# Optimization experiments

Hardware: AMD Instinct MI355X
Metric: run time of the kernel (lower is better)

Reference implementation:

```python
import jax, jax.numpy as jnp
import numpy as np

TEMPERATURE = 0.5
B, D = 4096, 256

def setup_inputs() -> dict:
    key = jax.random.key(0)
    k1, k2 = jax.random.split(key)
    z_i = jax.random.normal(k1, (B, D), dtype=jnp.float32)
    z_j = jax.random.normal(k2, (B, D), dtype=jnp.float32)
    return {"z_i": z_i, "z_j": z_j}

def reference(z_i, z_j):
    # NT-Xent loss (SimCLR). Cosine similarity of L2-normalized rows == dot product.
    b = z_i.shape[0]
    n = 2 * b
    zi = z_i / jnp.linalg.norm(z_i, axis=1, keepdims=True)
    zj = z_j / jnp.linalg.norm(z_j, axis=1, keepdims=True)
    z = jnp.concatenate([zi, zj], axis=0)            # [N, D]
    sim = jnp.matmul(z, z.T)                          # [N, N] cosine-sim matrix
    # positives: sim(i, i+b) and sim(i+b, i)
    pos = jnp.concatenate([jnp.diagonal(sim, offset=b), jnp.diagonal(sim, offset=-b)])  # [N]
    logits = sim / TEMPERATURE
    # Cross-entropy with the positive as the target class over {pos} U negatives.
    # The candidate set per row is all j != i (the positive j = partner(i) is included,
    # only the self-similarity diagonal is excluded) -> mask diagonal with -inf.
    neg_inf = jnp.asarray(-jnp.inf, dtype=logits.dtype)
    masked = jnp.where(jnp.eye(n, dtype=bool), neg_inf, logits)
    lse = jax.nn.logsumexp(masked, axis=1)            # [N]
    loss = jnp.sum(lse - pos / TEMPERATURE) / n
    return loss
```

## Files before the change

### kernel.cpp

```cpp
#include <hip/hip_runtime.h>
#include <hip/hip_bf16.h>


constexpr int BB = 4096;
constexpr int NN = 8192;
constexpr int DD = 256;
constexpr int TS = 128;
constexpr int NT = NN / TS;
constexpr int NBLK = NT * (NT + 1) / 2;
constexpr int KSTEPS = DD / 16;

typedef _Float16 half4v __attribute__((ext_vector_type(4)));
typedef _Float16 half8v __attribute__((ext_vector_type(8)));
typedef float floatx16 __attribute__((ext_vector_type(16)));

__global__ __launch_bounds__(256) void nt_normalize(
    const float* __restrict__ zi, const float* __restrict__ zj,
    _Float16* __restrict__ Zf, float* __restrict__ pos,
    float* __restrict__ rowsum)
{
    __shared__ _Float16 sZ[2][16 * 64 * 8];
    const int tid = threadIdx.x;
    const int pr  = tid >> 3;
    const int sub = tid & 7;
    const int p   = blockIdx.x * 32 + pr;

    if (blockIdx.x < 32) rowsum[blockIdx.x * 256 + tid] = 0.f;

    const float4* ai = (const float4*)(zi + (size_t)p * DD);
    const float4* bj = (const float4*)(zj + (size_t)p * DD);
    float4 av[8], bv[8];
    float ssi = 0.f, ssj = 0.f, dd = 0.f;
#pragma unroll
    for (int t = 0; t < 8; ++t) {
        av[t] = ai[sub + 8 * t];
        bv[t] = bj[sub + 8 * t];
        ssi += av[t].x*av[t].x + av[t].y*av[t].y + av[t].z*av[t].z + av[t].w*av[t].w;
        ssj += bv[t].x*bv[t].x + bv[t].y*bv[t].y + bv[t].z*bv[t].z + bv[t].w*bv[t].w;
        dd  += av[t].x*bv[t].x + av[t].y*bv[t].y + av[t].z*bv[t].z + av[t].w*bv[t].w;
    }
#pragma unroll
    for (int off = 1; off < 8; off <<= 1) {
        ssi += __shfl_xor(ssi, off);
        ssj += __shfl_xor(ssj, off);
        dd  += __shfl_xor(dd,  off);
    }
    const float invi = rsqrtf(ssi);
    const float invj = rsqrtf(ssj);
    if (sub == 0) pos[p] = dd * invi * invj;

#pragma unroll
    for (int t = 0; t < 8; ++t) {
        const int gi = (2 * t + (sub >> 2)) * 64 + pr + 32 * ((sub >> 1) & 1);
        const int wo = 4 * (sub & 1);
        half4v hi, hj;
        hi.x = (_Float16)(av[t].x * invi); hi.y = (_Float16)(av[t].y * invi);
        hi.z = (_Float16)(av[t].z * invi); hi.w = (_Float16)(av[t].w * invi);
        hj.x = (_Float16)(bv[t].x * invj); hj.y = (_Float16)(bv[t].y * invj);
        hj.z = (_Float16)(bv[t].z * invj); hj.w = (_Float16)(bv[t].w * invj);
        *(half4v*)&sZ[0][gi * 8 + wo] = hi;
        *(half4v*)&sZ[1][gi * 8 + wo] = hj;
    }
    __syncthreads();

    float4* Zf4 = (float4*)Zf;
    const float4* s0 = (const float4*)sZ[0];
    const float4* s1 = (const float4*)sZ[1];
    const size_t gbi = (size_t)blockIdx.x * 1024;
    const size_t gbj = (size_t)(128 + blockIdx.x) * 1024;
#pragma unroll
    for (int it = 0; it < 4; ++it) {
        Zf4[gbi + tid + it * 256] = s0[tid + it * 256];
        Zf4[gbj + tid + it * 256] = s1[tid + it * 256];
    }
}

__device__ __forceinline__ float half_sums(float x) {
    int t;
    t = __builtin_amdgcn_update_dpp(0, __builtin_bit_cast(int, x), 0x111, 0xf, 0xf, false);
    x += __builtin_bit_cast(float, t);
    t = __builtin_amdgcn_update_dpp(0, __builtin_bit_cast(int, x), 0x112, 0xf, 0xf, false);
    x += __builtin_bit_cast(float, t);
    t = __builtin_amdgcn_update_dpp(0, __builtin_bit_cast(int, x), 0x114, 0xf, 0xf, false);
    x += __builtin_bit_cast(float, t);
    t = __builtin_amdgcn_update_dpp(0, __builtin_bit_cast(int, x), 0x118, 0xf, 0xf, false);
    x += __builtin_bit_cast(float, t);
    t = __builtin_amdgcn_update_dpp(0, __builtin_bit_cast(int, x), 0x142, 0xa, 0xf, false);
    x += __builtin_bit_cast(float, t);
    return x;
}

__global__ __launch_bounds__(256, 4) void nt_simexp(
    const _Float16* __restrict__ Zf, float* __restrict__ rowsum)
{
    __shared__ float colacc[TS];

    const int bid = (blockIdx.x & 7) * (NBLK / 8) + (blockIdx.x >> 3);

    const int t = NBLK - 1 - bid;
    int m = (int)((sqrtf((float)(8 * t + 1)) - 1.0f) * 0.5f);
    while ((m + 1) * (m + 2) / 2 <= t) ++m;
    while (m * (m + 1) / 2 > t) --m;
    const int rt = NT - 1 - m;
    const int ct = NT - 1 - (t - m * (m + 1) / 2);
    const bool diag = (rt == ct);

    const int tid = threadIdx.x;
    const int wave = tid >> 6;
    const int lane = tid & 63;
    const int lm = lane & 31;
    const int lh = lane >> 5;
    const int wr = wave >> 1;
    const int wc = wave & 1;

    const int rbase = rt * TS;
    const int cbase = ct * TS;

    if (tid < TS) colacc[tid] = 0.f;
    __syncthreads();

    const int ga0 = (rbase >> 5) + wr * 2;
    const int gb0 = (cbase >> 5) + wc * 2;
    const half8v* pa0 = (const half8v*)Zf + (size_t)ga0 * 1024 + lane;
    const half8v* pa1 = pa0 + 1024;
    const half8v* pb0 = (const half8v*)Zf + (size_t)gb0 * 1024 + lane;
    const half8v* pb1 = pb0 + 1024;

    floatx16 a00, a01, a10, a11;
#pragma unroll
    for (int r = 0; r < 16; ++r) { a00[r] = 0.f; a01[r] = 0.f; a10[r] = 0.f; a11[r] = 0.f; }

    half8v fa0 = pa0[0], fa1 = pa1[0], fb0 = pb0[0], fb1 = pb1[0];
#pragma unroll
    for (int ks = 0; ks < KSTEPS; ++ks) {
        half8v na0 = fa0, na1 = fa1, nb0 = fb0, nb1 = fb1;
        if (ks + 1 < KSTEPS) {
            na0 = pa0[(ks + 1) * 64];
            na1 = pa1[(ks + 1) * 64];
            nb0 = pb0[(ks + 1) * 64];
            nb1 = pb1[(ks + 1) * 64];
        }
        a00 = __builtin_amdgcn_mfma_f32_32x32x16_f16(fa0, fb0, a00, 0, 0, 0);
        a01 = __builtin_amdgcn_mfma_f32_32x32x16_f16(fa0, fb1, a01, 0, 0, 0);
        a10 = __builtin_amdgcn_mfma_f32_32x32x16_f16(fa1, fb0, a10, 0, 0, 0);
        a11 = __builtin_amdgcn_mfma_f32_32x32x16_f16(fa1, fb1, a11, 0, 0, 0);
        fa0 = na0; fa1 = na1; fb0 = nb0; fb1 = nb1;
    }

    const float KEXP = 2.0f * 1.44269504088896340736f;
    float eb0 = 0.f, eb1 = 0.f;
#pragma unroll
    for (int tr = 0; tr < 2; ++tr) {
#pragma unroll
        for (int r = 0; r < 16; ++r) {
            const int mrow = (r & 3) + 8 * (r >> 2) + 4 * lh;
            float e0 = __builtin_amdgcn_exp2f((tr ? a10[r] : a00[r]) * KEXP);
            float e1 = __builtin_amdgcn_exp2f((tr ? a11[r] : a01[r]) * KEXP);
            if (diag && (wr == wc) && (mrow == lm)) {
                if (tr == 0) e0 = 0.f; else e1 = 0.f;
            }
            eb0 += e0; eb1 += e1;
            if (!diag) {
                float s2 = half_sums(e0 + e1);
                if (lm == 31)
                    atomicAdd(&colacc[wr * 64 + tr * 32 + mrow], s2);
            }
        }
    }

    eb0 += __shfl_xor(eb0, 32);
    eb1 += __shfl_xor(eb1, 32);
    if (lane < 32) {
        atomicAdd(&rowsum[cbase + wc * 64 + lm], eb0);
        atomicAdd(&rowsum[cbase + wc * 64 + 32 + lm], eb1);
    }
    if (!diag) {
        __syncthreads();
        if (tid < TS) atomicAdd(&rowsum[rbase + tid], colacc[tid]);
    }
}

__global__ __launch_bounds__(256) void nt_finalize(
    const float* __restrict__ rowsum, const float* __restrict__ pos,
    float* __restrict__ out)
{
    const int tid = threadIdx.x;
    float acc = 0.f;
#pragma unroll
    for (int it = 0; it < NN / 256; ++it)
        acc += __builtin_amdgcn_logf(rowsum[tid + it * 256]);
    float pacc = 0.f;
#pragma unroll
    for (int it = 0; it < BB / 256; ++it)
        pacc += pos[tid + it * 256];

#pragma unroll
    for (int off = 32; off > 0; off >>= 1) {
        acc  += __shfl_xor(acc,  off);
        pacc += __shfl_xor(pacc, off);
    }
    __shared__ float sa[4], sp[4];
    const int wave = tid >> 6;
    if ((tid & 63) == 0) { sa[wave] = acc; sp[wave] = pacc; }
    __syncthreads();
    if (tid == 0) {
        const float lntot = (sa[0] + sa[1] + sa[2] + sa[3]) * 0.6931471805599453f;
        const float ptot  = sp[0] + sp[1] + sp[2] + sp[3];
        out[0] = (lntot - 4.0f * ptot) * (1.0f / (float)NN);
    }
}

extern "C" void kernel_launch(void* const* d_in, const int* in_sizes, int n_in,
                              void* d_out, int out_size, void* d_ws, size_t ws_size,
                              hipStream_t stream) {
    const float* zi = (const float*)d_in[0];
    const float* zj = (const float*)d_in[1];
    float* out = (float*)d_out;

    _Float16* Zf = (_Float16*)d_ws;
    float* rowsum = (float*)((char*)d_ws + (size_t)NN * DD * 2);
    float* pos = rowsum + NN;

    nt_normalize<<<BB / 32, 256, 0, stream>>>(zi, zj, Zf, pos, rowsum);
    nt_simexp<<<NBLK, 256, 0, stream>>>((const _Float16*)Zf, rowsum);
    nt_finalize<<<1, 256, 0, stream>>>(rowsum, pos, out);
}
```

Measured before the change: 91.67 us.

## Stage row tile in LDS and sweep column chunks per block

Each block now loads a 128-row A tile into shared memory with global_load_lds. It then loops over up to eight column tiles of the upper triangle, with each wave computing a 128x64 strip, so A is reused across many column tiles instead of being reloaded from global memory for every 128x128 tile. Row-side partial sums are accumulated in shared memory and flushed once per block, which cuts global atomics. In exchange the grid shrinks to 288 blocks with uneven work (row chunks near the end are shorter), and register pressure rises with eight 32x32 accumulators per wave, hence the lower launch-bounds occupancy.

```diff
diff --git a/kernel.cpp b/kernel.cpp
--- a/kernel.cpp
+++ b/kernel.cpp
@@ -7,7 +7,8 @@
 constexpr int DD = 256;
 constexpr int TS = 128;
 constexpr int NT = NN / TS;
-constexpr int NBLK = NT * (NT + 1) / 2;
+constexpr int CW = 8;
+constexpr int NBLK = 288;
 constexpr int KSTEPS = DD / 16;
 
 typedef _Float16 half4v __attribute__((ext_vector_type(4)));
@@ -90,94 +91,118 @@
     return x;
 }
 
-__global__ __launch_bounds__(256, 4) void nt_simexp(
+__global__ __launch_bounds__(256, 2) void nt_simexp(
     const _Float16* __restrict__ Zf, float* __restrict__ rowsum)
 {
-    __shared__ float colacc[TS];
+    __shared__ alignas(16) _Float16 sA[4 * 16 * 64 * 8];
+    __shared__ float rowaccA[TS];
 
     const int bid = (blockIdx.x & 7) * (NBLK / 8) + (blockIdx.x >> 3);
 
-    const int t = NBLK - 1 - bid;
-    int m = (int)((sqrtf((float)(8 * t + 1)) - 1.0f) * 0.5f);
-    while ((m + 1) * (m + 2) / 2 <= t) ++m;
-    while (m * (m + 1) / 2 > t) --m;
-    const int rt = NT - 1 - m;
-    const int ct = NT - 1 - (t - m * (m + 1) / 2);
-    const bool diag = (rt == ct);
+    int rt = 0, rem = bid;
+    while (true) {
+        const int nch = (NT - rt + CW - 1) >> 3;
+        if (rem < nch) break;
+        rem -= nch; ++rt;
+    }
+    const int ct0 = rt + rem * CW;
+    const int ncw = min(CW, NT - ct0);
+    const int njobs = 2 * ncw;
 
     const int tid = threadIdx.x;
     const int wave = tid >> 6;
     const int lane = tid & 63;
     const int lm = lane & 31;
     const int lh = lane >> 5;
-    const int wr = wave >> 1;
-    const int wc = wave & 1;
-
-    const int rbase = rt * TS;
-    const int cbase = ct * TS;
-
-    if (tid < TS) colacc[tid] = 0.f;
-    __syncthreads();
-
-    const int ga0 = (rbase >> 5) + wr * 2;
-    const int gb0 = (cbase >> 5) + wc * 2;
-    const half8v* pa0 = (const half8v*)Zf + (size_t)ga0 * 1024 + lane;
-    const half8v* pa1 = pa0 + 1024;
-    const half8v* pb0 = (const half8v*)Zf + (size_t)gb0 * 1024 + lane;
-    const half8v* pb1 = pb0 + 1024;
-
-    floatx16 a00, a01, a10, a11;
-#pragma unroll
-    for (int r = 0; r < 16; ++r) { a00[r] = 0.f; a01[r] = 0.f; a10[r] = 0.f; a11[r] = 0.f; }
-
-    half8v fa0 = pa0[0], fa1 = pa1[0], fb0 = pb0[0], fb1 = pb1[0];
-#pragma unroll
-    for (int ks = 0; ks < KSTEPS; ++ks) {
-        half8v na0 = fa0, na1 = fa1, nb0 = fb0, nb1 = fb1;
-        if (ks + 1 < KSTEPS) {
-            na0 = pa0[(ks + 1) * 64];
-            na1 = pa1[(ks + 1) * 64];
-            nb0 = pb0[(ks + 1) * 64];
-            nb1 = pb1[(ks + 1) * 64];
-        }
-        a00 = __builtin_amdgcn_mfma_f32_32x32x16_f16(fa0, fb0, a00, 0, 0, 0);
-        a01 = __builtin_amdgcn_mfma_f32_32x32x16_f16(fa0, fb1, a01, 0, 0, 0);
-        a10 = __builtin_amdgcn_mfma_f32_32x32x16_f16(fa1, fb0, a10, 0, 0, 0);
-        a11 = __builtin_amdgcn_mfma_f32_32x32x16_f16(fa1, fb1, a11, 0, 0, 0);
-        fa0 = na0; fa1 = na1; fb0 = nb0; fb1 = nb1;
-    }
-
+
+    {
+        const _Float16* src = Zf + ((size_t)(rt * 4 + wave) * 1024 + lane) * 8;
+        _Float16* dst = sA + (size_t)wave * 16 * 64 * 8;
+#pragma unroll
+        for (int ks = 0; ks < 16; ++ks) {
+            __builtin_amdgcn_global_load_lds(
+                (const __attribute__((address_space(1))) unsigned int*)(src + ks * 64 * 8),
+                (__attribute__((address_space(3))) unsigned int*)(dst + ks * 64 * 8),
+                16, 0, 0);
+        }
+    }
+    if (tid < TS) rowaccA[tid] = 0.f;
+    __syncthreads();
+
+    const half8v* sAf = (const half8v*)sA;
     const float KEXP = 2.0f * 1.44269504088896340736f;
-    float eb0 = 0.f, eb1 = 0.f;
-#pragma unroll
-    for (int tr = 0; tr < 2; ++tr) {
-#pragma unroll
-        for (int r = 0; r < 16; ++r) {
-            const int mrow = (r & 3) + 8 * (r >> 2) + 4 * lh;
-            float e0 = __builtin_amdgcn_exp2f((tr ? a10[r] : a00[r]) * KEXP);
-            float e1 = __builtin_amdgcn_exp2f((tr ? a11[r] : a01[r]) * KEXP);
-            if (diag && (wr == wc) && (mrow == lm)) {
-                if (tr == 0) e0 = 0.f; else e1 = 0.f;
+
+    for (int j = wave; j < njobs; j += 4) {
+        const int ct = ct0 + (j >> 1);
+        const int jit = j & 1;
+        const bool dj = (ct == rt);
+        const int cb = ct * TS + jit * 64;
+
+        const half8v* pb0 = (const half8v*)Zf + ((size_t)(cb >> 5)) * 1024 + lane;
+        const half8v* pb1 = pb0 + 1024;
+
+        floatx16 acc[4][2];
+#pragma unroll
+        for (int g = 0; g < 4; ++g)
+#pragma unroll
+            for (int c = 0; c < 2; ++c)
+#pragma unroll
+                for (int r = 0; r < 16; ++r) acc[g][c][r] = 0.f;
+
+        half8v fb0 = pb0[0], fb1 = pb1[0];
+#pragma unroll
+        for (int ks = 0; ks < KSTEPS; ++ks) {
+            half8v nb0 = fb0, nb1 = fb1;
+            if (ks + 1 < KSTEPS) {
+                nb0 = pb0[(ks + 1) * 64];
+                nb1 = pb1[(ks + 1) * 64];
             }
-            eb0 += e0; eb1 += e1;
-            if (!diag) {
-                float s2 = half_sums(e0 + e1);
-                if (lm == 31)
-                    atomicAdd(&colacc[wr * 64 + tr * 32 + mrow], s2);
+            half8v fa0 = sAf[(0 * 16 + ks) * 64 + lane];
+            half8v fa1 = sAf[(1 * 16 + ks) * 64 + lane];
+            half8v fa2 = sAf[(2 * 16 + ks) * 64 + lane];
+            half8v fa3 = sAf[(3 * 16 + ks) * 64 + lane];
+            acc[0][0] = __builtin_amdgcn_mfma_f32_32x32x16_f16(fa0, fb0, acc[0][0], 0, 0, 0);
+            acc[0][1] = __builtin_amdgcn_mfma_f32_32x32x16_f16(fa0, fb1, acc[0][1], 0, 0, 0);
+            acc[1][0] = __builtin_amdgcn_mfma_f32_32x32x16_f16(fa1, fb0, acc[1][0], 0, 0, 0);
+            acc[1][1] = __builtin_amdgcn_mfma_f32_32x32x16_f16(fa1, fb1, acc[1][1], 0, 0, 0);
+            acc[2][0] = __builtin_amdgcn_mfma_f32_32x32x16_f16(fa2, fb0, acc[2][0], 0, 0, 0);
+            acc[2][1] = __builtin_amdgcn_mfma_f32_32x32x16_f16(fa2, fb1, acc[2][1], 0, 0, 0);
+            acc[3][0] = __builtin_amdgcn_mfma_f32_32x32x16_f16(fa3, fb0, acc[3][0], 0, 0, 0);
+            acc[3][1] = __builtin_amdgcn_mfma_f32_32x32x16_f16(fa3, fb1, acc[3][1], 0, 0, 0);
+            fb0 = nb0; fb1 = nb1;
+        }
+
+        float ebs0 = 0.f, ebs1 = 0.f;
+#pragma unroll
+        for (int g = 0; g < 4; ++g) {
+#pragma unroll
+            for (int r = 0; r < 16; ++r) {
+                const int mrow = (r & 3) + 8 * (r >> 2) + 4 * lh;
+                float e0 = __builtin_amdgcn_exp2f(acc[g][0][r] * KEXP);
+                float e1 = __builtin_amdgcn_exp2f(acc[g][1][r] * KEXP);
+                if (dj) {
+                    const int rowInTile = 32 * g + mrow;
+                    if (rowInTile == jit * 64 + lm)      e0 = 0.f;
+                    if (rowInTile == jit * 64 + 32 + lm) e1 = 0.f;
+                }
+                ebs0 += e0; ebs1 += e1;
+                if (!dj) {
+                    float s2 = half_sums(e0 + e1);
+                    if (lm == 31)
+                        atomicAdd(&rowaccA[32 * g + mrow], s2);
+                }
             }
         }
-    }
-
-    eb0 += __shfl_xor(eb0, 32);
-    eb1 += __shfl_xor(eb1, 32);
-    if (lane < 32) {
-        atomicAdd(&rowsum[cbase + wc * 64 + lm], eb0);
-        atomicAdd(&rowsum[cbase + wc * 64 + 32 + lm], eb1);
-    }
-    if (!diag) {
-        __syncthreads();
-        if (tid < TS) atomicAdd(&rowsum[rbase + tid], colacc[tid]);
-    }
+        ebs0 += __shfl_xor(ebs0, 32);
+        ebs1 += __shfl_xor(ebs1, 32);
+        if (lane < 32) {
+            atomicAdd(&rowsum[cb + lm], ebs0);
+            atomicAdd(&rowsum[cb + 32 + lm], ebs1);
+        }
+    }
+
+    __syncthreads();
+    if (tid < TS) atomicAdd(&rowsum[rt * TS + tid], rowaccA[tid]);
 }
 
 __global__ __launch_bounds__(256) void nt_finalize(
```

Result: slower. 160.2 us (+74.8%).
